# Kernel tuning notes

Measured on AMD Instinct MI355X. Metric: run time of the kernel, lower is better.

Reference implementation:

```python
import jax, jax.numpy as jnp
import numpy as np

IOU_T = 0.5          # iou_threshold
SCORE_T = 0.5        # score_threshold
MAX_OUT = 100        # max_output_boxes_per_class


def setup_inputs() -> dict:
    key = jax.random.key(0)
    k1, k2, k3 = jax.random.split(key, 3)
    B, C, N = 1, 80, 1024
    # boxes in y1x1y2x2 with positive extents (realistic detector outputs)
    mins = jax.random.uniform(k1, (B, N, 2), jnp.float32) * 100.0
    sizes = jax.random.uniform(k2, (B, N, 2), jnp.float32) * 50.0 + 1.0
    boxes = jnp.concatenate([mins, mins + sizes], axis=-1)  # [B, N, 4]
    scores = jax.random.uniform(k3, (B, C, N), jnp.float32)  # [B, C, N]
    return {"boxes": boxes, "scores": scores}


def _pairwise_iou(b):
    # b: [N,4] in y1x1y2x2 (IoU is invariant to the module's axis swap)
    y1, x1, y2, x2 = b[:, 0], b[:, 1], b[:, 2], b[:, 3]
    area = (y2 - y1) * (x2 - x1)
    ih = jnp.clip(jnp.minimum(y2[:, None], y2[None, :]) - jnp.maximum(y1[:, None], y1[None, :]), 0.0)
    iw = jnp.clip(jnp.minimum(x2[:, None], x2[None, :]) - jnp.maximum(x1[:, None], x1[None, :]), 0.0)
    inter = ih * iw
    return inter / (area[:, None] + area[None, :] - inter)


def _nms_one_class(boxes, scores):
    # boxes: [N,4], scores: [N] -> (idx:[MAX_OUT] kept original indices, -1 pad; valid:[MAX_OUT])
    N = scores.shape[0]
    order = jnp.argsort(-scores)              # descending score, matches torchvision.nms
    iou = _pairwise_iou(boxes[order])         # [N,N] in sorted order
    keep = scores[order] > SCORE_T            # score filter folded into initial keep mask
    js = jnp.arange(N)

    def body(i, keep):
        suppress = (iou[i] > IOU_T) & (js > i)
        return jnp.where(keep[i], keep & ~suppress, keep)

    keep = jax.lax.fori_loop(0, N, body, keep)
    rank = jnp.cumsum(keep) - 1               # output slot for each kept box
    slots = jnp.where(keep, jnp.clip(rank, 0, MAX_OUT), MAX_OUT)  # MAX_OUT = discard slot
    res = jnp.full((MAX_OUT + 1,), -1, jnp.int32).at[slots].set(order.astype(jnp.int32))
    idx = res[:MAX_OUT]
    return idx, idx >= 0


def reference(boxes, scores):
    B, C = scores.shape[0], scores.shape[1]
    nms_bc = jax.vmap(jax.vmap(_nms_one_class, in_axes=(None, 0)), in_axes=(0, 0))
    idx, valid = nms_bc(boxes, scores)        # [B,C,MAX_OUT]
    b_idx = jnp.broadcast_to(jnp.arange(B, dtype=jnp.int32)[:, None, None], (B, C, MAX_OUT))
    c_idx = jnp.broadcast_to(jnp.arange(C, dtype=jnp.int32)[None, :, None], (B, C, MAX_OUT))
    rows = jnp.stack([b_idx, c_idx, idx], axis=-1).reshape(-1, 3)  # [B*C*MAX_OUT, 3]
    v = valid.reshape(-1)
    total = B * C * MAX_OUT
    # pack valid rows contiguously at the front (mirrors torch's put_ on a zeros buffer)
    pos = jnp.where(v, jnp.cumsum(v.astype(jnp.int32)) - 1, total)
    out = jnp.zeros((total, 3), jnp.int32).at[pos].set(rows, mode='drop')
    return out
```

## Files before the change

### kernel.cpp

```cpp
#include <hip/hip_runtime.h>
#include <stdint.h>

#define N_BOX 1024
#define NUM_CLASSES 80
#define MAX_OUT 100
#define KEPT_STRIDE 128
#define WS_POISON 0xAAAAAAAAu

__device__ __forceinline__ void cas64(unsigned long long& a, unsigned long long& b, bool desc) {
    bool sw = desc ? (a < b) : (a > b);
    unsigned long long t = a;
    a = sw ? b : a;
    b = sw ? t : b;
}

__global__ __launch_bounds__(256) void nms_fused(const float* __restrict__ boxes,
                                                 const float* __restrict__ scores,
                                                 int* __restrict__ keptIdx,
                                                 unsigned int* __restrict__ counts,
                                                 unsigned int* __restrict__ ready,
                                                 int* __restrict__ out) {
    __shared__ float4 sbox[N_BOX];
    __shared__ float sarea[N_BOX];
    __shared__ unsigned long long keys[N_BOX];
    __shared__ float4 kbox[MAX_OUT];
    __shared__ float karea[MAX_OUT];
    __shared__ int scnt[NUM_CLASSES];
    const int c = blockIdx.x;
    const int tid = threadIdx.x;
    const int lane = tid & 63;

    for (int i = tid; i < N_BOX; i += 256) {
        float4 b = reinterpret_cast<const float4*>(boxes)[i];
        sbox[i] = b;
        sarea[i] = (b.z - b.x) * (b.w - b.y);
    }

    const float* sc = scores + (size_t)c * N_BOX;
    float4 s4 = reinterpret_cast<const float4*>(sc)[tid];
    const int i0 = tid * 4;
    unsigned long long K[4];
    K[0] = ((unsigned long long)__float_as_uint(s4.x) << 32) | (unsigned long long)(0xFFFFFFFFu - (unsigned)(i0 + 0));
    K[1] = ((unsigned long long)__float_as_uint(s4.y) << 32) | (unsigned long long)(0xFFFFFFFFu - (unsigned)(i0 + 1));
    K[2] = ((unsigned long long)__float_as_uint(s4.z) << 32) | (unsigned long long)(0xFFFFFFFFu - (unsigned)(i0 + 2));
    K[3] = ((unsigned long long)__float_as_uint(s4.w) << 32) | (unsigned long long)(0xFFFFFFFFu - (unsigned)(i0 + 3));

    auto shfl_pass = [&](int j, bool d) {
        int xl = j >> 2;
        bool mx = (d == ((lane & xl) == 0));
#pragma unroll
        for (int t = 0; t < 4; ++t) {
            unsigned long long p = __shfl_xor(K[t], xl, 64);
            K[t] = mx ? (K[t] >= p ? K[t] : p) : (K[t] <= p ? K[t] : p);
        }
    };
    auto thread_pass = [&](bool d) {
        cas64(K[0], K[2], d); cas64(K[1], K[3], d);
        cas64(K[0], K[1], d); cas64(K[2], K[3], d);
    };
    auto lds_pass = [&](int j, bool d) {
        *reinterpret_cast<ulonglong2*>(&keys[i0])     = make_ulonglong2(K[0], K[1]);
        *reinterpret_cast<ulonglong2*>(&keys[i0 + 2]) = make_ulonglong2(K[2], K[3]);
        __syncthreads();
        int pb = i0 ^ j;
        ulonglong2 p01 = *reinterpret_cast<const ulonglong2*>(&keys[pb]);
        ulonglong2 p23 = *reinterpret_cast<const ulonglong2*>(&keys[pb + 2]);
        unsigned long long P[4] = {p01.x, p01.y, p23.x, p23.y};
        bool mx = (d == ((i0 & j) == 0));
#pragma unroll
        for (int t = 0; t < 4; ++t)
            K[t] = mx ? (K[t] >= P[t] ? K[t] : P[t]) : (K[t] <= P[t] ? K[t] : P[t]);
        __syncthreads();
    };

    cas64(K[0], K[1], true);
    cas64(K[2], K[3], false);
    { bool d = (tid & 1) == 0; thread_pass(d); }
    for (int k = 8; k <= 256; k <<= 1) {
        bool d = (tid & (k >> 2)) == 0;
        for (int j = k >> 1; j >= 4; j >>= 1) shfl_pass(j, d);
        thread_pass(d);
    }
    { bool d = (tid & 128) == 0;
      lds_pass(256, d);
      for (int j = 128; j >= 4; j >>= 1) shfl_pass(j, d);
      thread_pass(d); }
    {
      lds_pass(512, true); lds_pass(256, true);
      for (int j = 128; j >= 4; j >>= 1) shfl_pass(j, true);
      thread_pass(true); }
    *reinterpret_cast<ulonglong2*>(&keys[i0])     = make_ulonglong2(K[0], K[1]);
    *reinterpret_cast<ulonglong2*>(&keys[i0 + 2]) = make_ulonglong2(K[2], K[3]);
    __syncthreads();

    if (tid < 64) {
        int kept = 0;
        int* outc = keptIdx + c * KEPT_STRIDE;
        for (int base = 0; base < N_BOX && kept < MAX_OUT; base += 64) {
            unsigned long long kk = keys[base + lane];
            unsigned int hi = (unsigned int)(kk >> 32);
            unsigned int o = 0xFFFFFFFFu - (unsigned int)kk;
            bool valid = hi > 0x3F000000u;
            if (__ballot(valid) == 0ull) break;
            float4 mb = sbox[o];
            float ma = sarea[o];
            bool alive = valid;
            for (int j = 0; j < kept; ++j) {
                float4 kb = kbox[j];
                float ih = fminf(kb.z, mb.z) - fmaxf(kb.x, mb.x); ih = fmaxf(ih, 0.0f);
                float iw = fminf(kb.w, mb.w) - fmaxf(kb.y, mb.y); iw = fmaxf(iw, 0.0f);
                float inter = ih * iw;
                float uni = karea[j] + ma - inter;
                alive = alive && !((inter / uni) > 0.5f);
            }
            unsigned long long m = __ballot(alive);
            if (m == 0ull) continue;
            unsigned long long row = 0ull;
#pragma unroll 8
            for (int j = 0; j < 64; ++j) {
                unsigned int oj = (unsigned int)__shfl((int)o, j);
                float4 bj = sbox[oj];
                float aj = sarea[oj];
                float ih = fminf(bj.z, mb.z) - fmaxf(bj.x, mb.x); ih = fmaxf(ih, 0.0f);
                float iw = fminf(bj.w, mb.w) - fmaxf(bj.y, mb.y); iw = fmaxf(iw, 0.0f);
                float inter = ih * iw;
                float uni = aj + ma - inter;
                if ((inter / uni) > 0.5f) row |= 1ull << j;
            }
            unsigned long long Km = 0ull;
            int kept0 = kept;
            while (m != 0ull && kept < MAX_OUT) {
                int f = __builtin_ctzll(m);
                Km |= 1ull << f;
                ++kept;
                unsigned int rlo = (unsigned int)__builtin_amdgcn_readlane((int)(unsigned int)row, f);
                unsigned int rhi = (unsigned int)__builtin_amdgcn_readlane((int)(unsigned int)(row >> 32), f);
                unsigned long long rowf = ((unsigned long long)rhi << 32) | rlo;
                m &= ~rowf;
            }
            if ((Km >> lane) & 1ull) {
                int pos = kept0 + __popcll(Km & ((1ull << lane) - 1ull));
                outc[pos] = (int)o;
                kbox[pos] = mb;
                karea[pos] = ma;
            }
        }
        if (lane == 0) {
            __hip_atomic_store(&counts[c], (unsigned int)kept,
                               __ATOMIC_RELEASE, __HIP_MEMORY_SCOPE_SYSTEM);
            __hip_atomic_fetch_add(ready, 1u,
                                   __ATOMIC_RELEASE, __HIP_MEMORY_SCOPE_SYSTEM);
        }
    }

    if (c != 0) return;

    if (tid == 64) {
        const unsigned int target = WS_POISON + (unsigned int)NUM_CLASSES;
        unsigned int v;
        do {
            v = __hip_atomic_fetch_add(ready, 0u, __ATOMIC_ACQUIRE, __HIP_MEMORY_SCOPE_SYSTEM);
        } while (v != target);
    } else if (tid >= 144) {
        int4* o4 = reinterpret_cast<int4*>(out);
        for (int i = tid - 144; i < (NUM_CLASSES * MAX_OUT * 3) / 4; i += 112)
            o4[i] = make_int4(0, 0, 0, 0);
    }
    __syncthreads();

    if (tid < NUM_CLASSES)
        scnt[tid] = (int)__hip_atomic_load(&counts[tid], __ATOMIC_RELAXED,
                                           __HIP_MEMORY_SCOPE_SYSTEM);
    __syncthreads();

    for (int d = 1; d < NUM_CLASSES; d <<= 1) {
        int v = 0;
        if (tid < NUM_CLASSES) {
            v = scnt[tid];
            if (tid >= d) v += scnt[tid - d];
        }
        __syncthreads();
        if (tid < NUM_CLASSES) scnt[tid] = v;
        __syncthreads();
    }

    for (int idx = tid; idx < NUM_CLASSES * MAX_OUT; idx += 256) {
        int c2 = idx / MAX_OUT;
        int r = idx - c2 * MAX_OUT;
        int excl = (c2 == 0) ? 0 : scnt[c2 - 1];
        if (r < scnt[c2] - excl) {
            int o = excl + r;
            out[o * 3 + 0] = 0;
            out[o * 3 + 1] = c2;
            out[o * 3 + 2] = keptIdx[c2 * KEPT_STRIDE + r];
        }
    }
}

extern "C" void kernel_launch(void* const* d_in, const int* in_sizes, int n_in,
                              void* d_out, int out_size, void* d_ws, size_t ws_size,
                              hipStream_t stream) {
    const float* boxes = (const float*)d_in[0];
    const float* scores = (const float*)d_in[1];
    int* out = (int*)d_out;

    int* keptIdx = (int*)d_ws;
    unsigned int* counts = (unsigned int*)(keptIdx + NUM_CLASSES * KEPT_STRIDE);
    unsigned int* ready = counts + 128;

    nms_fused<<<NUM_CLASSES, 256, 0, stream>>>(boxes, scores, keptIdx, counts, ready, out);
}
```

Measured before the change: 99.83 us.

## Spread greedy NMS suppression work across all four wavefronts of the block

The greedy NMS stage used to run on a single wavefront while the other three idled. Now all four wavefronts split the check of each 64-candidate chunk against the kept boxes, and each computes 16 columns of the in-chunk IoU matrix. Partial masks are combined through shared memory, and wave 0 still runs the serial resolve. The cost is three extra __syncthreads per chunk and more shared-memory traffic.

```diff
diff --git a/kernel.cpp b/kernel.cpp
--- a/kernel.cpp
+++ b/kernel.cpp
@@ -25,10 +25,14 @@
     __shared__ unsigned long long keys[N_BOX];
     __shared__ float4 kbox[MAX_OUT];
     __shared__ float karea[MAX_OUT];
+    __shared__ unsigned long long supp[4];
+    __shared__ unsigned long long wmp[4][64];
+    __shared__ int keptLDS;
     __shared__ int scnt[NUM_CLASSES];
     const int c = blockIdx.x;
     const int tid = threadIdx.x;
     const int lane = tid & 63;
+    const int wv = tid >> 6;
 
     for (int i = tid; i < N_BOX; i += 256) {
         float4 b = reinterpret_cast<const float4*>(boxes)[i];
@@ -85,15 +89,15 @@
       lds_pass(256, d);
       for (int j = 128; j >= 4; j >>= 1) shfl_pass(j, d);
       thread_pass(d); }
-    {
-      lds_pass(512, true); lds_pass(256, true);
+    { lds_pass(512, true); lds_pass(256, true);
       for (int j = 128; j >= 4; j >>= 1) shfl_pass(j, true);
       thread_pass(true); }
     *reinterpret_cast<ulonglong2*>(&keys[i0])     = make_ulonglong2(K[0], K[1]);
     *reinterpret_cast<ulonglong2*>(&keys[i0 + 2]) = make_ulonglong2(K[2], K[3]);
+    if (tid == 0) keptLDS = 0;
     __syncthreads();
 
-    if (tid < 64) {
+    {
         int kept = 0;
         int* outc = keptIdx + c * KEPT_STRIDE;
         for (int base = 0; base < N_BOX && kept < MAX_OUT; base += 64) {
@@ -101,51 +105,67 @@
             unsigned int hi = (unsigned int)(kk >> 32);
             unsigned int o = 0xFFFFFFFFu - (unsigned int)kk;
             bool valid = hi > 0x3F000000u;
-            if (__ballot(valid) == 0ull) break;
+            unsigned long long vb = __ballot(valid);
+            if (vb == 0ull) break;
             float4 mb = sbox[o];
             float ma = sarea[o];
-            bool alive = valid;
-            for (int j = 0; j < kept; ++j) {
+            bool sup_part = false;
+            for (int j = wv; j < kept; j += 4) {
                 float4 kb = kbox[j];
                 float ih = fminf(kb.z, mb.z) - fmaxf(kb.x, mb.x); ih = fmaxf(ih, 0.0f);
                 float iw = fminf(kb.w, mb.w) - fmaxf(kb.y, mb.y); iw = fmaxf(iw, 0.0f);
                 float inter = ih * iw;
                 float uni = karea[j] + ma - inter;
-                alive = alive && !((inter / uni) > 0.5f);
+                sup_part = sup_part || ((inter / uni) > 0.5f);
             }
-            unsigned long long m = __ballot(alive);
-            if (m == 0ull) continue;
-            unsigned long long row = 0ull;
-#pragma unroll 8
-            for (int j = 0; j < 64; ++j) {
-                unsigned int oj = (unsigned int)__shfl((int)o, j);
-                float4 bj = sbox[oj];
-                float aj = sarea[oj];
-                float ih = fminf(bj.z, mb.z) - fmaxf(bj.x, mb.x); ih = fmaxf(ih, 0.0f);
-                float iw = fminf(bj.w, mb.w) - fmaxf(bj.y, mb.y); iw = fmaxf(iw, 0.0f);
-                float inter = ih * iw;
-                float uni = aj + ma - inter;
-                if ((inter / uni) > 0.5f) row |= 1ull << j;
+            unsigned long long sb = __ballot(sup_part);
+            if (lane == 0) supp[wv] = sb;
+            __syncthreads();
+            unsigned long long m = vb & ~(supp[0] | supp[1] | supp[2] | supp[3]);
+            bool doM = (m != 0ull);
+            if (doM) {
+                unsigned long long chunk = 0ull;
+#pragma unroll
+                for (int jj = 0; jj < 16; ++jj) {
+                    int j = (wv << 4) + jj;
+                    unsigned long long kj = keys[base + j];
+                    unsigned int oj = 0xFFFFFFFFu - (unsigned int)kj;
+                    float4 bj = sbox[oj];
+                    float aj = sarea[oj];
+                    float ih = fminf(bj.z, mb.z) - fmaxf(bj.x, mb.x); ih = fmaxf(ih, 0.0f);
+                    float iw = fminf(bj.w, mb.w) - fmaxf(bj.y, mb.y); iw = fmaxf(iw, 0.0f);
+                    float inter = ih * iw;
+                    float uni = aj + ma - inter;
+                    if ((inter / uni) > 0.5f) chunk |= 1ull << jj;
+                }
+                wmp[wv][lane] = chunk << (wv << 4);
             }
-            unsigned long long Km = 0ull;
-            int kept0 = kept;
-            while (m != 0ull && kept < MAX_OUT) {
-                int f = __builtin_ctzll(m);
-                Km |= 1ull << f;
-                ++kept;
-                unsigned int rlo = (unsigned int)__builtin_amdgcn_readlane((int)(unsigned int)row, f);
-                unsigned int rhi = (unsigned int)__builtin_amdgcn_readlane((int)(unsigned int)(row >> 32), f);
-                unsigned long long rowf = ((unsigned long long)rhi << 32) | rlo;
-                m &= ~rowf;
+            __syncthreads();
+            if (doM && tid < 64) {
+                unsigned long long row = wmp[0][lane] | wmp[1][lane] | wmp[2][lane] | wmp[3][lane];
+                unsigned long long Km = 0ull;
+                int kept0 = kept;
+                while (m != 0ull && kept < MAX_OUT) {
+                    int f = __builtin_ctzll(m);
+                    Km |= 1ull << f;
+                    ++kept;
+                    unsigned int rlo = (unsigned int)__builtin_amdgcn_readlane((int)(unsigned int)row, f);
+                    unsigned int rhi = (unsigned int)__builtin_amdgcn_readlane((int)(unsigned int)(row >> 32), f);
+                    unsigned long long rowf = ((unsigned long long)rhi << 32) | rlo;
+                    m &= ~rowf;
+                }
+                if ((Km >> lane) & 1ull) {
+                    int pos = kept0 + __popcll(Km & ((1ull << lane) - 1ull));
+                    outc[pos] = (int)o;
+                    kbox[pos] = mb;
+                    karea[pos] = ma;
+                }
+                if (lane == 0) keptLDS = kept;
             }
-            if ((Km >> lane) & 1ull) {
-                int pos = kept0 + __popcll(Km & ((1ull << lane) - 1ull));
-                outc[pos] = (int)o;
-                kbox[pos] = mb;
-                karea[pos] = ma;
-            }
-        }
-        if (lane == 0) {
+            __syncthreads();
+            kept = keptLDS;
+        }
+        if (tid == 0) {
             __hip_atomic_store(&counts[c], (unsigned int)kept,
                                __ATOMIC_RELEASE, __HIP_MEMORY_SCOPE_SYSTEM);
             __hip_atomic_fetch_add(ready, 1u,
```

Measured after the change: 89.36 us. 10.5% less time.
